# Kernel tuning notes

Hardware: AMD Instinct MI355X
Metric: run time of the kernel (lower is better)

## Reference

```python
import jax, jax.numpy as jnp
import numpy as np

B, S, V, CTX, NC, D, NH, L, FF, MAXS = 8, 512, 32000, 8, 512, 256, 4, 4, 512, 512
PAD = 0  # ram_model.pad_token_id


def setup_inputs() -> dict:
    key = jax.random.key(0)
    ks = iter(jax.random.split(key, 64))
    def p(shape, s=0.02):
        return jax.random.normal(next(ks), shape, jnp.float32) * s
    inp = {}
    inp["token_ids"] = jax.random.randint(next(ks), (B, S), 0, V)
    inp["ram_table"] = p((V, NC), 0.1)          # frozen RAM per-cluster scores
    inp["proj_W"] = p((NC, D)); inp["proj_b"] = jnp.zeros((D,), jnp.float32)
    inp["pos_emb"] = p((MAXS, D))
    for pre in ("sa", "ca"):
        for nm in ("Wq", "Wk", "Wv", "Wo"):
            inp[f"{pre}_{nm}"] = p((L, D, D))
        for nm in ("bq", "bk", "bv", "bo"):
            inp[f"{pre}_{nm}"] = jnp.zeros((L, D), jnp.float32)
    for i in (1, 2, 3):
        inp[f"ln{i}_s"] = jnp.ones((L, D), jnp.float32)
        inp[f"ln{i}_b"] = jnp.zeros((L, D), jnp.float32)
    inp["ff_W1"] = p((L, D, FF)); inp["ff_b1"] = jnp.zeros((L, FF), jnp.float32)
    inp["ff_W2"] = p((L, FF, D)); inp["ff_b2"] = jnp.zeros((L, D), jnp.float32)
    inp["out_W"] = p((D, V)); inp["out_b"] = jnp.zeros((V,), jnp.float32)
    return inp


def _ln(x, s, b):
    m = x.mean(-1, keepdims=True)
    v = ((x - m) ** 2).mean(-1, keepdims=True)
    return (x - m) * jax.lax.rsqrt(v + 1e-5) * s + b


def _mha(q_in, k_in, v_in, Wq, bq, Wk, bk, Wv, bv, Wo, bo, mask):
    b, sq, d = q_in.shape
    hd = d // NH
    q = (q_in @ Wq + bq).reshape(b, sq, NH, hd)
    k = (k_in @ Wk + bk).reshape(b, -1, NH, hd)
    v = (v_in @ Wv + bv).reshape(b, -1, NH, hd)
    sc = jnp.einsum("bqhd,bkhd->bhqk", q, k) / np.sqrt(hd).astype(np.float32)
    if mask is not None:
        sc = jnp.where(mask, -1e9, sc)  # mask broadcast over [b, h]
    a = jax.nn.softmax(sc, axis=-1)
    o = jnp.einsum("bhqk,bkhd->bqhd", a, v).reshape(b, sq, d)
    return o @ Wo + bo


def _forward(token_ids, ram_table, proj_W, proj_b, pos_emb,
             sa_Wq, sa_bq, sa_Wk, sa_bk, sa_Wv, sa_bv, sa_Wo, sa_bo,
             ca_Wq, ca_bq, ca_Wk, ca_bk, ca_Wv, ca_bv, ca_Wo, ca_bo,
             ln1_s, ln1_b, ln2_s, ln2_b, ln3_s, ln3_b,
             ff_W1, ff_b1, ff_W2, ff_b2, out_W, out_b):
    b, s = token_ids.shape
    # Batched sliding context windows (replaces the per-position Python loop):
    # left-pad with PAD so window at pos covers [pos-CTX+1, pos].
    padded = jnp.concatenate(
        [jnp.full((b, CTX - 1), PAD, token_ids.dtype), token_ids], axis=1)
    idx = jnp.arange(s)[:, None] + jnp.arange(CTX)[None, :]  # [S, CTX]
    win = padded[:, idx]                                      # [B, S, CTX]
    # Frozen RAM feature extraction: per-cluster scores averaged over window.
    scores = ram_table[win].mean(axis=2)                      # [B, S, NC]
    x = scores @ proj_W + proj_b + pos_emb[:s]                # [B, S, D]
    mask = jnp.triu(jnp.ones((s, s), bool), 1)                # causal
    mem = jnp.zeros((b, 1, D), x.dtype)
    for l in range(L):
        h = _ln(x, ln1_s[l], ln1_b[l])
        x = x + _mha(h, h, h, sa_Wq[l], sa_bq[l], sa_Wk[l], sa_bk[l],
                     sa_Wv[l], sa_bv[l], sa_Wo[l], sa_bo[l], mask)
        h = _ln(x, ln2_s[l], ln2_b[l])
        x = x + _mha(h, mem, mem, ca_Wq[l], ca_bq[l], ca_Wk[l], ca_bk[l],
                     ca_Wv[l], ca_bv[l], ca_Wo[l], ca_bo[l], None)
        h = _ln(x, ln3_s[l], ln3_b[l])
        x = x + jax.nn.relu(h @ ff_W1[l] + ff_b1[l]) @ ff_W2[l] + ff_b2[l]
    return x @ out_W + out_b                                  # [B, S, V]


def reference(token_ids, ram_table, proj_W, proj_b, pos_emb,
              sa_Wq, sa_bq, sa_Wk, sa_bk, sa_Wv, sa_bv, sa_Wo, sa_bo,
              ca_Wq, ca_bq, ca_Wk, ca_bk, ca_Wv, ca_bv, ca_Wo, ca_bo,
              ln1_s, ln1_b, ln2_s, ln2_b, ln3_s, ln3_b,
              ff_W1, ff_b1, ff_W2, ff_b2, out_W, out_b):
    return _forward(token_ids, ram_table, proj_W, proj_b, pos_emb,
                    sa_Wq, sa_bq, sa_Wk, sa_bk, sa_Wv, sa_bv, sa_Wo, sa_bo,
                    ca_Wq, ca_bq, ca_Wk, ca_bk, ca_Wv, ca_bv, ca_Wo, ca_bo,
                    ln1_s, ln1_b, ln2_s, ln2_b, ln3_s, ln3_b,
                    ff_W1, ff_b1, ff_W2, ff_b2, out_W, out_b)
```

## Files before the change

### kernel.cpp

```cpp
#include <hip/hip_runtime.h>

#define B_   8
#define S_   512
#define V_   32000
#define CTX_ 8
#define NC_  512
#define D_   256
#define NH_  4
#define L_   4
#define FF_  512
#define HD_  64
#define BS_  4096

#define FG_F32   1
#define FG_BF16  2
#define FG_RELU  4
#define FG_POS   8
#define FG_NT    16
#define FG_QKV   32

typedef __attribute__((ext_vector_type(8))) short bf16x8;
typedef __attribute__((ext_vector_type(4))) float f32x4;

__device__ inline void gload16(const void* g, void* lds) {
    __builtin_amdgcn_global_load_lds(
        (const __attribute__((address_space(1))) void*)g,
        (__attribute__((address_space(3))) void*)lds, 16, 0, 0);
}

__device__ inline ushort f2b(float f) {
    union { float f; unsigned u; } v; v.f = f;
    unsigned u = v.u;
    unsigned r = u + 0x7fffu + ((u >> 16) & 1u);
    return (ushort)(r >> 16);
}

__global__ __launch_bounds__(256) void embed_bf16_kernel(
    const int* __restrict__ tok, const float* __restrict__ table,
    ushort* __restrict__ scores)
{
    int bs = blockIdx.x;
    int b = bs >> 9, s = bs & 511;
    int j = threadIdx.x;
    float a0 = 0.f, a1 = 0.f;
    #pragma unroll
    for (int c = 0; c < CTX_; ++c) {
        int pos = s + c - (CTX_ - 1);
        int t = (pos < 0) ? 0 : tok[b * S_ + pos];
        const float* row = table + (size_t)t * NC_;
        a0 += row[j];
        a1 += row[j + 256];
    }
    scores[(size_t)bs * NC_ + j]       = f2b(a0 * 0.125f);
    scores[(size_t)bs * NC_ + j + 256] = f2b(a1 * 0.125f);
}

__global__ __launch_bounds__(256) void ln_bf16_kernel(
    const float* __restrict__ x, const float* __restrict__ sc,
    const float* __restrict__ bi, ushort* __restrict__ out)
{
    int row = blockIdx.x * 4 + (threadIdx.x >> 6);
    int lane = threadIdx.x & 63;
    float4 v = *reinterpret_cast<const float4*>(x + (size_t)row * D_ + lane * 4);
    float s = v.x + v.y + v.z + v.w;
    float s2 = v.x * v.x + v.y * v.y + v.z * v.z + v.w * v.w;
    #pragma unroll
    for (int o = 32; o > 0; o >>= 1) {
        s  += __shfl_xor(s, o);
        s2 += __shfl_xor(s2, o);
    }
    float mean = s * (1.f / D_);
    float var = s2 * (1.f / D_) - mean * mean;
    float r = rsqrtf(var + 1e-5f);
    float4 g = *reinterpret_cast<const float4*>(sc + lane * 4);
    float4 bb = *reinterpret_cast<const float4*>(bi + lane * 4);
    ushort4 o4;
    o4.x = f2b((v.x - mean) * r * g.x + bb.x);
    o4.y = f2b((v.y - mean) * r * g.y + bb.y);
    o4.z = f2b((v.z - mean) * r * g.z + bb.z);
    o4.w = f2b((v.w - mean) * r * g.w + bb.w);
    *reinterpret_cast<ushort4*>(out + (size_t)row * D_ + lane * 4) = o4;
}

__global__ __launch_bounds__(1024) void setup_kernel(
    const float* __restrict__ ca_bv, const float* __restrict__ ca_Wo,
    const float* __restrict__ ca_bo, float* __restrict__ cc,
    const float* __restrict__ bq, const float* __restrict__ bk,
    const float* __restrict__ bv, float* __restrict__ qkvb)
{
    int l = blockIdx.x, t = threadIdx.x;
    if (t < 256) {
        const float* w = ca_Wo + (size_t)l * D_ * D_;
        const float* b = ca_bv + l * D_;
        float acc = 0.f;
        for (int d = 0; d < D_; ++d) acc += b[d] * w[(size_t)d * D_ + t];
        cc[l * D_ + t] = acc + ca_bo[l * D_ + t];
    } else {
        int u = t - 256;
        int which = u >> 8, c = u & 255;
        const float* src = which == 0 ? bq : which == 1 ? bk : bv;
        qkvb[l * 768 + u] = src[l * 256 + c];
    }
}

__global__ void transpose_all_kernel(
    const float* __restrict__ proj_W, const float* __restrict__ Wq,
    const float* __restrict__ Wk, const float* __restrict__ Wv,
    const float* __restrict__ Wo, const float* __restrict__ W1,
    const float* __restrict__ W2, const float* __restrict__ outW,
    ushort* __restrict__ pjWb, ushort* __restrict__ WqkvB,
    ushort* __restrict__ WoB, ushort* __restrict__ ff1B,
    ushort* __restrict__ ff2B, ushort* __restrict__ Wb)
{
    int id = blockIdx.x;
    const float* src; ushort* dst; int K, N, lt;
    if (id < 128)       { src = proj_W; dst = pjWb; K = 512; N = 256; lt = id; }
    else if (id < 896)  { lt = id - 128; int z = lt >> 6; lt &= 63;
                          int which = z / L_, l = z % L_;
                          src = (which == 0 ? Wq : which == 1 ? Wk : Wv) + (size_t)l * 65536;
                          dst = WqkvB + ((size_t)l * 768 + which * 256) * 256;
                          K = 256; N = 256; }
    else if (id < 1152) { lt = id - 896; int l = lt >> 6; lt &= 63;
                          src = Wo + (size_t)l * 65536; dst = WoB + (size_t)l * 65536;
                          K = 256; N = 256; }
    else if (id < 1664) { lt = id - 1152; int l = lt >> 7; lt &= 127;
                          src = W1 + (size_t)l * 131072; dst = ff1B + (size_t)l * 131072;
                          K = 256; N = 512; }
    else if (id < 2176) { lt = id - 1664; int l = lt >> 7; lt &= 127;
                          src = W2 + (size_t)l * 131072; dst = ff2B + (size_t)l * 131072;
                          K = 512; N = 256; }
    else                { lt = id - 2176; src = outW; dst = Wb; K = 256; N = 32000; }
    int ntc = N >> 5;
    int n0 = (lt % ntc) * 32, k0 = (lt / ntc) * 32;
    __shared__ float tile[32][33];
    for (int i = threadIdx.y; i < 32; i += 8)
        tile[i][threadIdx.x] = src[(size_t)(k0 + i) * N + n0 + threadIdx.x];
    __syncthreads();
    for (int i = threadIdx.y; i < 32; i += 8)
        dst[(size_t)(n0 + i) * K + k0 + threadIdx.x] = f2b(tile[threadIdx.x][i]);
}

template<int BM, int BN, int K, int TN, int FLAGS>
__global__ __launch_bounds__(256) void gemm_t(
    const ushort* __restrict__ A, const ushort* __restrict__ Bt,
    const float* __restrict__ bias, const float* __restrict__ extra,
    const float* __restrict__ resid, const float* __restrict__ pos,
    float* __restrict__ Cf, ushort* __restrict__ Cb)
{
    constexpr int WM = BM / 32;
    constexpr int WN = BN / 32;
    constexpr int MT = 4096 / BM;
    constexpr int NWG = MT * (TN / BN);
    __shared__ ushort smem[(BM + BN) * 64];
    ushort* As = smem;
    ushort* Bs = smem + BM * 64;
    int bid = blockIdx.x;
    int swz = bid;
    if constexpr ((NWG & 7) == 0) {
        constexpr int cpx = NWG >> 3;
        swz = (bid & 7) * cpx + (bid >> 3);
    }
    int mt = swz % MT, nt = swz / MT;
    int row0 = mt * BM, col0 = nt * BN;
    int t = threadIdx.x, w = t >> 6, lane = t & 63;
    int wr = w >> 1, wc = w & 1;
    int srow = lane >> 3, slot = lane & 7;
    int gcol = (slot ^ srow) * 8;

    f32x4 acc[WM][WN] = {};
    int sl = lane >> 4;
    int rA0 = wr * (BM / 2) + (lane & 15);
    int rB0 = wc * (BN / 2) + (lane & 15);

    #pragma unroll
    for (int k0 = 0; k0 < K; k0 += 64) {
        #pragma unroll
        for (int c = 0; c < BM / 32; ++c) {
            int chunk = w * (BM / 32) + c;
            gload16(A + (size_t)(row0 + chunk * 8 + srow) * K + k0 + gcol,
                    As + chunk * 512);
        }
        #pragma unroll
        for (int c = 0; c < BN / 32; ++c) {
            int chunk = w * (BN / 32) + c;
            gload16(Bt + (size_t)(col0 + chunk * 8 + srow) * K + k0 + gcol,
                    Bs + chunk * 512);
        }
        __syncthreads();
        #pragma unroll
        for (int kk = 0; kk < 2; ++kk) {
            bf16x8 a[WM], b[WN];
            #pragma unroll
            for (int m = 0; m < WM; ++m) {
                int rr = rA0 + m * 16;
                a[m] = *reinterpret_cast<const bf16x8*>(
                    As + rr * 64 + (((sl + kk * 4) ^ (rr & 7)) * 8));
            }
            #pragma unroll
            for (int n = 0; n < WN; ++n) {
                int rr = rB0 + n * 16;
                b[n] = *reinterpret_cast<const bf16x8*>(
                    Bs + rr * 64 + (((sl + kk * 4) ^ (rr & 7)) * 8));
            }
            #pragma unroll
            for (int m = 0; m < WM; ++m)
                #pragma unroll
                for (int n = 0; n < WN; ++n)
                    acc[m][n] = __builtin_amdgcn_mfma_f32_16x16x32_bf16(
                        a[m], b[n], acc[m][n], 0, 0, 0);
        }
        __syncthreads();
    }

    int lr = (lane >> 4) * 4;
    int lc = lane & 15;

    if constexpr (FLAGS & FG_NT) {
        float* Ct = reinterpret_cast<float*>(smem);
        #pragma unroll
        for (int p = 0; p < 2; ++p) {
            __syncthreads();
            if (wr == p) {
                #pragma unroll
                for (int n = 0; n < WN; ++n) {
                    int colL = wc * (BN / 2) + n * 16 + lc;
                    float bn = bias[col0 + colL];
                    #pragma unroll
                    for (int m = 0; m < WM; ++m)
                        #pragma unroll
                        for (int r = 0; r < 4; ++r)
                            Ct[(m * 16 + lr + r) * BN + colL] = acc[m][n][r] + bn;
                }
            }
            __syncthreads();
            constexpr int NV4 = (BM / 2) * (BN / 4);
            #pragma unroll
            for (int j = 0; j < NV4 / 256; ++j) {
                int idx = t + j * 256;
                int rl = idx / (BN / 4);
                int c4 = idx % (BN / 4);
                f32x4 v4 = reinterpret_cast<const f32x4*>(Ct)[idx];
                __builtin_nontemporal_store(v4,
                    reinterpret_cast<f32x4*>(
                        &Cf[(size_t)(row0 + p * (BM / 2) + rl) * TN + col0 + c4 * 4]));
            }
        }
        return;
    }

    #pragma unroll
    for (int n = 0; n < WN; ++n) {
        int col = col0 + wc * (BN / 2) + n * 16 + lc;
        float bn = bias ? bias[col] : 0.f;
        float en = extra ? extra[col] : 0.f;
        #pragma unroll
        for (int m = 0; m < WM; ++m) {
            int rbase = row0 + wr * (BM / 2) + m * 16 + lr;
            #pragma unroll
            for (int r = 0; r < 4; ++r) {
                int row = rbase + r;
                float v = acc[m][n][r] + bn;
                if constexpr (FLAGS & FG_QKV) {
                    int which = col >> 8;
                    int c2 = col & 255;
                    int hh = c2 >> 6, dd = c2 & 63;
                    int bb = row >> 9, ss = row & 511;
                    if (which == 0) {
                        Cb[((((size_t)bb * NH_ + hh) * S_ + ss) << 6) + dd] =
                            f2b(v * 0.125f);
                    } else if (which == 1) {
                        (Cb + 1048576)[((((size_t)bb * NH_ + hh) * S_ + ss) << 6) + dd] =
                            f2b(v);
                    } else {
                        (Cb + 2097152)[((((size_t)bb * NH_ + hh) * HD_ + dd) << 9) + ss] =
                            f2b(v);
                    }
                } else {
                    if constexpr (FLAGS & FG_POS) v += pos[(size_t)(row & 511) * TN + col];
                    if (extra) v += en;
                    if (resid) v += resid[(size_t)row * TN + col];
                    if constexpr (FLAGS & FG_RELU) v = fmaxf(v, 0.f);
                    if constexpr (FLAGS & FG_BF16)
                        Cb[(size_t)row * TN + col] = f2b(v);
                    if constexpr (FLAGS & FG_F32)
                        Cf[(size_t)row * TN + col] = v;
                }
            }
        }
    }
}

__global__ __launch_bounds__(256) void attn_kernel(
    const ushort* __restrict__ q, const ushort* __restrict__ k,
    const ushort* __restrict__ vT, ushort* __restrict__ pv)
{
    int qt = blockIdx.x, bh = blockIdx.y;
    __shared__ ushort Ks[64 * 64];
    __shared__ ushort Vs[64 * 64];
    __shared__ ushort Ps[4 * 16 * 64];
    int t = threadIdx.x, w = t >> 6, lane = t & 63;
    int srow = lane >> 3, slot = lane & 7;
    int gcol = (slot ^ srow) * 8;
    int sl = lane >> 4, lc = lane & 15;

    const ushort* Qp = q + ((size_t)bh * S_ + qt * 64) * HD_;
    const ushort* Kp = k + (size_t)bh * S_ * HD_;
    const ushort* Vp = vT + (size_t)bh * HD_ * S_;

    int qrow = w * 16 + lc;
    bf16x8 qf0 = *reinterpret_cast<const bf16x8*>(Qp + qrow * 64 + sl * 8);
    bf16x8 qf1 = *reinterpret_cast<const bf16x8*>(Qp + qrow * 64 + sl * 8 + 32);

    f32x4 o[4] = {};
    float m_r[4], l_r[4];
    #pragma unroll
    for (int r = 0; r < 4; ++r) { m_r[r] = -1e30f; l_r[r] = 0.f; }
    int row_abs = qt * 64 + w * 16 + sl * 4;

    for (int kt = 0; kt <= qt; ++kt) {
        #pragma unroll
        for (int c = 0; c < 2; ++c) {
            int chunk = w * 2 + c;
            gload16(Kp + (size_t)(kt * 64 + chunk * 8 + srow) * 64 + gcol,
                    Ks + chunk * 512);
            gload16(Vp + (size_t)(chunk * 8 + srow) * 512 + kt * 64 + gcol,
                    Vs + chunk * 512);
        }
        __syncthreads();

        f32x4 sa[4] = {};
        #pragma unroll
        for (int n = 0; n < 4; ++n) {
            int rB = n * 16 + lc;
            bf16x8 b0 = *reinterpret_cast<const bf16x8*>(
                Ks + rB * 64 + ((sl ^ (rB & 7)) * 8));
            bf16x8 b1 = *reinterpret_cast<const bf16x8*>(
                Ks + rB * 64 + (((sl + 4) ^ (rB & 7)) * 8));
            sa[n] = __builtin_amdgcn_mfma_f32_16x16x32_bf16(qf0, b0, sa[n], 0, 0, 0);
            sa[n] = __builtin_amdgcn_mfma_f32_16x16x32_bf16(qf1, b1, sa[n], 0, 0, 0);
        }
        if (kt == qt) {
            #pragma unroll
            for (int n = 0; n < 4; ++n) {
                int col = kt * 64 + n * 16 + lc;
                #pragma unroll
                for (int r = 0; r < 4; ++r)
                    if (col > row_abs + r) sa[n][r] = -1e30f;
            }
        }
        float psum[4];
        #pragma unroll
        for (int r = 0; r < 4; ++r) {
            float vm = fmaxf(fmaxf(sa[0][r], sa[1][r]), fmaxf(sa[2][r], sa[3][r]));
            vm = fmaxf(vm, __shfl_xor(vm, 1));
            vm = fmaxf(vm, __shfl_xor(vm, 2));
            vm = fmaxf(vm, __shfl_xor(vm, 4));
            vm = fmaxf(vm, __shfl_xor(vm, 8));
            float mn = fmaxf(m_r[r], vm);
            float scl = __expf(m_r[r] - mn);
            m_r[r] = mn;
            l_r[r] *= scl;
            #pragma unroll
            for (int n = 0; n < 4; ++n) o[n][r] *= scl;
            psum[r] = 0.f;
        }
        ushort* Pw = Ps + w * 1024;
        #pragma unroll
        for (int n = 0; n < 4; ++n) {
            #pragma unroll
            for (int r = 0; r < 4; ++r) {
                float p = __expf(sa[n][r] - m_r[r]);
                psum[r] += p;
                int prow = sl * 4 + r;
                int pcol = n * 16 + lc;
                int pslot = pcol >> 3;
                Pw[prow * 64 + ((pslot ^ (prow & 7)) * 8) + (pcol & 7)] = f2b(p);
            }
        }
        #pragma unroll
        for (int r = 0; r < 4; ++r) {
            float s = psum[r];
            s += __shfl_xor(s, 1);
            s += __shfl_xor(s, 2);
            s += __shfl_xor(s, 4);
            s += __shfl_xor(s, 8);
            l_r[r] += s;
        }
        int arow = lc;
        bf16x8 pa0 = *reinterpret_cast<const bf16x8*>(
            Pw + arow * 64 + ((sl ^ (arow & 7)) * 8));
        bf16x8 pa1 = *reinterpret_cast<const bf16x8*>(
            Pw + arow * 64 + (((sl + 4) ^ (arow & 7)) * 8));
        #pragma unroll
        for (int n = 0; n < 4; ++n) {
            int rB = n * 16 + lc;
            bf16x8 v0 = *reinterpret_cast<const bf16x8*>(
                Vs + rB * 64 + ((sl ^ (rB & 7)) * 8));
            bf16x8 v1 = *reinterpret_cast<const bf16x8*>(
                Vs + rB * 64 + (((sl + 4) ^ (rB & 7)) * 8));
            o[n] = __builtin_amdgcn_mfma_f32_16x16x32_bf16(pa0, v0, o[n], 0, 0, 0);
            o[n] = __builtin_amdgcn_mfma_f32_16x16x32_bf16(pa1, v1, o[n], 0, 0, 0);
        }
        __syncthreads();
    }

    int bb = bh >> 2, hh = bh & 3;
    #pragma unroll
    for (int r = 0; r < 4; ++r) {
        float inv = 1.f / l_r[r];
        int ss = qt * 64 + w * 16 + sl * 4 + r;
        #pragma unroll
        for (int n = 0; n < 4; ++n) {
            int dd = n * 16 + lc;
            pv[((size_t)bb * S_ + ss) * D_ + hh * HD_ + dd] = f2b(o[n][r] * inv);
        }
    }
}

extern "C" void kernel_launch(void* const* d_in, const int* in_sizes, int n_in,
                              void* d_out, int out_size, void* d_ws, size_t ws_size,
                              hipStream_t stream)
{
    const int*   tok     = (const int*)  d_in[0];
    const float* ram     = (const float*)d_in[1];
    const float* proj_W  = (const float*)d_in[2];
    const float* proj_b  = (const float*)d_in[3];
    const float* pos_emb = (const float*)d_in[4];
    const float* sa_Wq   = (const float*)d_in[5];
    const float* sa_Wk   = (const float*)d_in[6];
    const float* sa_Wv   = (const float*)d_in[7];
    const float* sa_Wo   = (const float*)d_in[8];
    const float* sa_bq   = (const float*)d_in[9];
    const float* sa_bk   = (const float*)d_in[10];
    const float* sa_bv   = (const float*)d_in[11];
    const float* sa_bo   = (const float*)d_in[12];
    const float* ca_Wo   = (const float*)d_in[16];
    const float* ca_bv   = (const float*)d_in[19];
    const float* ca_bo   = (const float*)d_in[20];
    const float* ln1_s   = (const float*)d_in[21];
    const float* ln1_b   = (const float*)d_in[22];
    const float* ln3_s   = (const float*)d_in[25];
    const float* ln3_b   = (const float*)d_in[26];
    const float* ff_W1   = (const float*)d_in[27];
    const float* ff_b1   = (const float*)d_in[28];
    const float* ff_W2   = (const float*)d_in[29];
    const float* ff_b2   = (const float*)d_in[30];
    const float* out_W   = (const float*)d_in[31];
    const float* out_b   = (const float*)d_in[32];

    float* out = (float*)d_out;
    float* ws  = (float*)d_ws;

    float*  x   = ws;
    float*  cc  = ws + (size_t)BS_ * D_;
    ushort* xb  = (ushort*)(cc + L_ * D_);
    ushort* Wb  = xb + (size_t)BS_ * D_;

    ushort* sc_b  = (ushort*)out;
    ushort* h_b   = sc_b + 2097152;
    ushort* qkv3  = h_b + 1048576;
    ushort* pv_b  = qkv3 + 3145728;
    ushort* ffh_b = pv_b + 1048576;
    ushort* pjWb  = ffh_b + 2097152;
    ushort* WqkvB = pjWb + 131072;
    ushort* WoB   = WqkvB + 786432;
    ushort* ff1B  = WoB + 262144;
    ushort* ff2B  = ff1B + 524288;
    float*  qkvb  = (float*)(ff2B + 524288);
    ushort* qb_b  = qkv3;
    ushort* kb_b  = qkv3 + 1048576;
    ushort* vT_b  = qkv3 + 2097152;

    setup_kernel<<<L_, 1024, 0, stream>>>(ca_bv, ca_Wo, ca_bo, cc,
                                          sa_bq, sa_bk, sa_bv, qkvb);
    embed_bf16_kernel<<<BS_, 256, 0, stream>>>(tok, ram, sc_b);
    transpose_all_kernel<<<10176, dim3(32, 8), 0, stream>>>(
        proj_W, sa_Wq, sa_Wk, sa_Wv, sa_Wo, ff_W1, ff_W2, out_W,
        pjWb, WqkvB, WoB, ff1B, ff2B, Wb);

    gemm_t<64, 64, 512, 256, FG_F32 | FG_POS><<<256, 256, 0, stream>>>(
        sc_b, pjWb, proj_b, nullptr, nullptr, pos_emb, x, nullptr);

    for (int l = 0; l < L_; ++l) {
        ln_bf16_kernel<<<1024, 256, 0, stream>>>(x, ln1_s + l * D_, ln1_b + l * D_, h_b);
        gemm_t<64, 64, 256, 768, FG_QKV><<<768, 256, 0, stream>>>(
            h_b, WqkvB + (size_t)l * 196608, qkvb + l * 768,
            nullptr, nullptr, nullptr, nullptr, qkv3);
        attn_kernel<<<dim3(8, 32), 256, 0, stream>>>(qb_b, kb_b, vT_b, pv_b);
        gemm_t<64, 64, 256, 256, FG_F32><<<256, 256, 0, stream>>>(
            pv_b, WoB + (size_t)l * 65536, sa_bo + l * D_,
            cc + l * D_, x, nullptr, x, nullptr);
        ln_bf16_kernel<<<1024, 256, 0, stream>>>(x, ln3_s + l * D_, ln3_b + l * D_, h_b);
        gemm_t<64, 64, 256, 512, FG_BF16 | FG_RELU><<<512, 256, 0, stream>>>(
            h_b, ff1B + (size_t)l * 131072, ff_b1 + l * FF_,
            nullptr, nullptr, nullptr, nullptr, ffh_b);
        if (l < L_ - 1) {
            gemm_t<64, 64, 512, 256, FG_F32><<<256, 256, 0, stream>>>(
                ffh_b, ff2B + (size_t)l * 131072, ff_b2 + l * D_,
                nullptr, x, nullptr, x, nullptr);
        } else {
            gemm_t<64, 64, 512, 256, FG_BF16><<<256, 256, 0, stream>>>(
                ffh_b, ff2B + (size_t)l * 131072, ff_b2 + l * D_,
                nullptr, x, nullptr, nullptr, xb);
        }
    }

    gemm_t<128, 128, 256, 32000, FG_F32 | FG_NT><<<8000, 256, 0, stream>>>(
        xb, Wb, out_b, nullptr, nullptr, nullptr, out, nullptr);
}
```

Measured before the change: 416.7 us.

## Merge prologue kernels into one launch and double-buffer K/V tiles in attention

Merges the setup, embedding and weight-transpose kernels into a single prologue launch, with block ranges dispatched by block index, which removes two launches and lets the independent work share the GPU. The attention kernel now double-buffers its K/V shared-memory tiles, prefetching the next tile while computing on the current one, and drops the trailing barrier. This raises LDS use per block and relies on the single remaining barrier per iteration to keep the buffers from racing.

```diff
diff --git a/kernel.cpp b/kernel.cpp
--- a/kernel.cpp
+++ b/kernel.cpp
@@ -35,24 +35,77 @@
     return (ushort)(r >> 16);
 }
 
-__global__ __launch_bounds__(256) void embed_bf16_kernel(
-    const int* __restrict__ tok, const float* __restrict__ table,
+__global__ __launch_bounds__(256) void prologue_kernel(
+    const int* __restrict__ tok, const float* __restrict__ ram,
+    const float* __restrict__ proj_W, const float* __restrict__ Wq,
+    const float* __restrict__ Wk, const float* __restrict__ Wv,
+    const float* __restrict__ Wo, const float* __restrict__ W1,
+    const float* __restrict__ W2, const float* __restrict__ outW,
+    const float* __restrict__ ca_bv, const float* __restrict__ ca_Wo,
+    const float* __restrict__ ca_bo, const float* __restrict__ bq,
+    const float* __restrict__ bk, const float* __restrict__ bv,
+    ushort* __restrict__ pjWb, ushort* __restrict__ WqkvB,
+    ushort* __restrict__ WoB, ushort* __restrict__ ff1B,
+    ushort* __restrict__ ff2B, ushort* __restrict__ Wb,
+    float* __restrict__ cc, float* __restrict__ qkvb,
     ushort* __restrict__ scores)
 {
-    int bs = blockIdx.x;
-    int b = bs >> 9, s = bs & 511;
-    int j = threadIdx.x;
-    float a0 = 0.f, a1 = 0.f;
-    #pragma unroll
-    for (int c = 0; c < CTX_; ++c) {
-        int pos = s + c - (CTX_ - 1);
-        int t = (pos < 0) ? 0 : tok[b * S_ + pos];
-        const float* row = table + (size_t)t * NC_;
-        a0 += row[j];
-        a1 += row[j + 256];
-    }
-    scores[(size_t)bs * NC_ + j]       = f2b(a0 * 0.125f);
-    scores[(size_t)bs * NC_ + j + 256] = f2b(a1 * 0.125f);
+    __shared__ float tile[32 * 33];
+    int id = blockIdx.x;
+    int t = threadIdx.x;
+    if (id < 10176) {
+        const float* src; ushort* dst; int K, N, lt;
+        if (id < 128)       { src = proj_W; dst = pjWb; K = 512; N = 256; lt = id; }
+        else if (id < 896)  { lt = id - 128; int z = lt >> 6; lt &= 63;
+                              int which = z / L_, l = z % L_;
+                              src = (which == 0 ? Wq : which == 1 ? Wk : Wv) + (size_t)l * 65536;
+                              dst = WqkvB + ((size_t)l * 768 + which * 256) * 256;
+                              K = 256; N = 256; }
+        else if (id < 1152) { lt = id - 896; int l = lt >> 6; lt &= 63;
+                              src = Wo + (size_t)l * 65536; dst = WoB + (size_t)l * 65536;
+                              K = 256; N = 256; }
+        else if (id < 1664) { lt = id - 1152; int l = lt >> 7; lt &= 127;
+                              src = W1 + (size_t)l * 131072; dst = ff1B + (size_t)l * 131072;
+                              K = 256; N = 512; }
+        else if (id < 2176) { lt = id - 1664; int l = lt >> 7; lt &= 127;
+                              src = W2 + (size_t)l * 131072; dst = ff2B + (size_t)l * 131072;
+                              K = 512; N = 256; }
+        else                { lt = id - 2176; src = outW; dst = Wb; K = 256; N = 32000; }
+        int ntc = N >> 5;
+        int n0 = (lt % ntc) * 32, k0 = (lt / ntc) * 32;
+        int tx = t & 31, ty = t >> 5;
+        for (int i = ty; i < 32; i += 8)
+            tile[i * 33 + tx] = src[(size_t)(k0 + i) * N + n0 + tx];
+        __syncthreads();
+        for (int i = ty; i < 32; i += 8)
+            dst[(size_t)(n0 + i) * K + k0 + tx] = f2b(tile[tx * 33 + i]);
+    } else if (id < 10180) {
+        int l = id - 10176;
+        const float* w = ca_Wo + (size_t)l * D_ * D_;
+        const float* b = ca_bv + l * D_;
+        float acc = 0.f;
+        for (int d = 0; d < D_; ++d) acc += b[d] * w[(size_t)d * D_ + t];
+        cc[l * D_ + t] = acc + ca_bo[l * D_ + t];
+        for (int u = t; u < 768; u += 256) {
+            int which = u >> 8, c = u & 255;
+            const float* src = which == 0 ? bq : which == 1 ? bk : bv;
+            qkvb[l * 768 + u] = src[l * 256 + c];
+        }
+    } else {
+        int bs = id - 10180;
+        int b = bs >> 9, s = bs & 511;
+        float a0 = 0.f, a1 = 0.f;
+        #pragma unroll
+        for (int c = 0; c < CTX_; ++c) {
+            int pos = s + c - (CTX_ - 1);
+            int tk = (pos < 0) ? 0 : tok[b * S_ + pos];
+            const float* row = ram + (size_t)tk * NC_;
+            a0 += row[t];
+            a1 += row[t + 256];
+        }
+        scores[(size_t)bs * NC_ + t]       = f2b(a0 * 0.125f);
+        scores[(size_t)bs * NC_ + t + 256] = f2b(a1 * 0.125f);
+    }
 }
 
 __global__ __launch_bounds__(256) void ln_bf16_kernel(
@@ -80,64 +133,6 @@
     o4.z = f2b((v.z - mean) * r * g.z + bb.z);
     o4.w = f2b((v.w - mean) * r * g.w + bb.w);
     *reinterpret_cast<ushort4*>(out + (size_t)row * D_ + lane * 4) = o4;
-}
-
-__global__ __launch_bounds__(1024) void setup_kernel(
-    const float* __restrict__ ca_bv, const float* __restrict__ ca_Wo,
-    const float* __restrict__ ca_bo, float* __restrict__ cc,
-    const float* __restrict__ bq, const float* __restrict__ bk,
-    const float* __restrict__ bv, float* __restrict__ qkvb)
-{
-    int l = blockIdx.x, t = threadIdx.x;
-    if (t < 256) {
-        const float* w = ca_Wo + (size_t)l * D_ * D_;
-        const float* b = ca_bv + l * D_;
-        float acc = 0.f;
-        for (int d = 0; d < D_; ++d) acc += b[d] * w[(size_t)d * D_ + t];
-        cc[l * D_ + t] = acc + ca_bo[l * D_ + t];
-    } else {
-        int u = t - 256;
-        int which = u >> 8, c = u & 255;
-        const float* src = which == 0 ? bq : which == 1 ? bk : bv;
-        qkvb[l * 768 + u] = src[l * 256 + c];
-    }
-}
-
-__global__ void transpose_all_kernel(
-    const float* __restrict__ proj_W, const float* __restrict__ Wq,
-    const float* __restrict__ Wk, const float* __restrict__ Wv,
-    const float* __restrict__ Wo, const float* __restrict__ W1,
-    const float* __restrict__ W2, const float* __restrict__ outW,
-    ushort* __restrict__ pjWb, ushort* __restrict__ WqkvB,
-    ushort* __restrict__ WoB, ushort* __restrict__ ff1B,
-    ushort* __restrict__ ff2B, ushort* __restrict__ Wb)
-{
-    int id = blockIdx.x;
-    const float* src; ushort* dst; int K, N, lt;
-    if (id < 128)       { src = proj_W; dst = pjWb; K = 512; N = 256; lt = id; }
-    else if (id < 896)  { lt = id - 128; int z = lt >> 6; lt &= 63;
-                          int which = z / L_, l = z % L_;
-                          src = (which == 0 ? Wq : which == 1 ? Wk : Wv) + (size_t)l * 65536;
-                          dst = WqkvB + ((size_t)l * 768 + which * 256) * 256;
-                          K = 256; N = 256; }
-    else if (id < 1152) { lt = id - 896; int l = lt >> 6; lt &= 63;
-                          src = Wo + (size_t)l * 65536; dst = WoB + (size_t)l * 65536;
-                          K = 256; N = 256; }
-    else if (id < 1664) { lt = id - 1152; int l = lt >> 7; lt &= 127;
-                          src = W1 + (size_t)l * 131072; dst = ff1B + (size_t)l * 131072;
-                          K = 256; N = 512; }
-    else if (id < 2176) { lt = id - 1664; int l = lt >> 7; lt &= 127;
-                          src = W2 + (size_t)l * 131072; dst = ff2B + (size_t)l * 131072;
-                          K = 512; N = 256; }
-    else                { lt = id - 2176; src = outW; dst = Wb; K = 256; N = 32000; }
-    int ntc = N >> 5;
-    int n0 = (lt % ntc) * 32, k0 = (lt / ntc) * 32;
-    __shared__ float tile[32][33];
-    for (int i = threadIdx.y; i < 32; i += 8)
-        tile[i][threadIdx.x] = src[(size_t)(k0 + i) * N + n0 + threadIdx.x];
-    __syncthreads();
-    for (int i = threadIdx.y; i < 32; i += 8)
-        dst[(size_t)(n0 + i) * K + k0 + threadIdx.x] = f2b(tile[threadIdx.x][i]);
 }
 
 template<int BM, int BN, int K, int TN, int FLAGS>
@@ -295,9 +290,8 @@
     const ushort* __restrict__ vT, ushort* __restrict__ pv)
 {
     int qt = blockIdx.x, bh = blockIdx.y;
-    __shared__ ushort Ks[64 * 64];
-    __shared__ ushort Vs[64 * 64];
-    __shared__ ushort Ps[4 * 16 * 64];
+    __shared__ ushort smem[20480];
+    ushort* Ps = smem + 16384;
     int t = threadIdx.x, w = t >> 6, lane = t & 63;
     int srow = lane >> 3, slot = lane & 7;
     int gcol = (slot ^ srow) * 8;
@@ -317,16 +311,34 @@
     for (int r = 0; r < 4; ++r) { m_r[r] = -1e30f; l_r[r] = 0.f; }
     int row_abs = qt * 64 + w * 16 + sl * 4;
 
-    for (int kt = 0; kt <= qt; ++kt) {
+    {
+        ushort* Ks = smem;
+        ushort* Vs = smem + 4096;
         #pragma unroll
         for (int c = 0; c < 2; ++c) {
             int chunk = w * 2 + c;
-            gload16(Kp + (size_t)(kt * 64 + chunk * 8 + srow) * 64 + gcol,
-                    Ks + chunk * 512);
-            gload16(Vp + (size_t)(chunk * 8 + srow) * 512 + kt * 64 + gcol,
-                    Vs + chunk * 512);
-        }
+            gload16(Kp + (size_t)(chunk * 8 + srow) * 64 + gcol, Ks + chunk * 512);
+            gload16(Vp + (size_t)(chunk * 8 + srow) * 512 + gcol, Vs + chunk * 512);
+        }
+    }
+
+    for (int kt = 0; kt <= qt; ++kt) {
+        int cur = kt & 1;
+        ushort* Ks = smem + cur * 8192;
+        ushort* Vs = smem + cur * 8192 + 4096;
         __syncthreads();
+        if (kt < qt) {
+            ushort* Kn = smem + (cur ^ 1) * 8192;
+            ushort* Vn = Kn + 4096;
+            #pragma unroll
+            for (int c = 0; c < 2; ++c) {
+                int chunk = w * 2 + c;
+                gload16(Kp + (size_t)((kt + 1) * 64 + chunk * 8 + srow) * 64 + gcol,
+                        Kn + chunk * 512);
+                gload16(Vp + (size_t)(chunk * 8 + srow) * 512 + (kt + 1) * 64 + gcol,
+                        Vn + chunk * 512);
+            }
+        }
 
         f32x4 sa[4] = {};
         #pragma unroll
@@ -401,7 +413,6 @@
             o[n] = __builtin_amdgcn_mfma_f32_16x16x32_bf16(pa0, v0, o[n], 0, 0, 0);
             o[n] = __builtin_amdgcn_mfma_f32_16x16x32_bf16(pa1, v1, o[n], 0, 0, 0);
         }
-        __syncthreads();
     }
 
     int bb = bh >> 2, hh = bh & 3;
@@ -471,12 +482,10 @@
     ushort* kb_b  = qkv3 + 1048576;
     ushort* vT_b  = qkv3 + 2097152;
 
-    setup_kernel<<<L_, 1024, 0, stream>>>(ca_bv, ca_Wo, ca_bo, cc,
-                                          sa_bq, sa_bk, sa_bv, qkvb);
-    embed_bf16_kernel<<<BS_, 256, 0, stream>>>(tok, ram, sc_b);
-    transpose_all_kernel<<<10176, dim3(32, 8), 0, stream>>>(
-        proj_W, sa_Wq, sa_Wk, sa_Wv, sa_Wo, ff_W1, ff_W2, out_W,
-        pjWb, WqkvB, WoB, ff1B, ff2B, Wb);
+    prologue_kernel<<<14276, 256, 0, stream>>>(
+        tok, ram, proj_W, sa_Wq, sa_Wk, sa_Wv, sa_Wo, ff_W1, ff_W2, out_W,
+        ca_bv, ca_Wo, ca_bo, sa_bq, sa_bk, sa_bv,
+        pjWb, WqkvB, WoB, ff1B, ff2B, Wb, cc, qkvb, sc_b);
 
     gemm_t<64, 64, 512, 256, FG_F32 | FG_POS><<<256, 256, 0, stream>>>(
         sc_b, pjWb, proj_b, nullptr, nullptr, pos_emb, x, nullptr);
```

Result: faster. 400.0 us (-4.0%).
